# Kernel optimization log

Hardware: AMD Instinct MI355X
Metric: run time of the kernel (lower is better)

## Reference

```python
import jax, jax.numpy as jnp
import numpy as np

RBF_CO = 10.077141124806595


def setup_inputs() -> dict:
    key = jax.random.key(0)
    k1, k2, k3 = jax.random.split(key, 3)
    n, dim = 2048, 128
    N, out_dim = 50000, 64
    features = jax.random.normal(k1, (n, dim), dtype=jnp.float32)
    train_data = jax.random.normal(k2, (N, dim), dtype=jnp.float32)
    weights = jax.random.normal(k3, (N, out_dim), dtype=jnp.float32) * 0.02
    return {"features": features, "train_data": train_data, "weights": weights}


def reference(features, train_data, weights):
    x2 = jnp.sum(features * features, axis=-1, keepdims=True)      # [n, 1]
    t2 = jnp.sum(train_data * train_data, axis=-1)                 # [N]
    d2 = x2 + t2[None, :] - 2.0 * (features @ train_data.T)        # [n, N]
    dist = jnp.sqrt(jnp.maximum(d2, 0.0))                          # clamp fp error
    k = jnp.exp(-dist / RBF_CO / 2.0)                              # RBF kernel [n, N]
    return k @ weights                                              # [n, out_dim]
```

## Files before the change

kernel.cpp:

```cpp
#include <hip/hip_runtime.h>
#include <hip/hip_bf16.h>
#include <stdint.h>

#define DIM 128
#define ODIM 64
#define BM 128
#define BN 64
#define NSPLIT 64

typedef __attribute__((ext_vector_type(8))) __bf16 bf16x8;
typedef __attribute__((ext_vector_type(2))) __bf16 bf16x2;
typedef __attribute__((ext_vector_type(4))) float f32x4;

#define MFMA16(a, b, c) __builtin_amdgcn_mfma_f32_16x16x32_bf16((a), (b), (c), 0, 0, 0)

#define RBFD 10.077141124806595
#define LOG2E 1.4426950408889634
#define C2D ((LOG2E / (2.0 * RBFD)) * (LOG2E / (2.0 * RBFD)))

__device__ __forceinline__ void async_copy16(const void* g, void* l) {
  __builtin_amdgcn_global_load_lds((const __attribute__((address_space(1))) void*)g,
                                   (__attribute__((address_space(3))) void*)l, 16, 0, 0);
}

__device__ __forceinline__ uint32_t pack_bf16(float a, float b) {
  uint32_t ua = __builtin_bit_cast(uint32_t, a) + 0x8000u;
  uint32_t ub = __builtin_bit_cast(uint32_t, b) + 0x8000u;
  return __builtin_amdgcn_perm(ub, ua, 0x07060302u);
}

__global__ void prep_all(const float* __restrict__ train, __bf16* __restrict__ Tb,
                         float* __restrict__ t2, const float* __restrict__ feat,
                         __bf16* __restrict__ Fb, float* __restrict__ x2,
                         const float* __restrict__ W, __bf16* __restrict__ Wt,
                         int Ntrain, int Npad, int nFeat,
                         int trainBlocks, int rowBlocks, float scale, float tScale) {
  __shared__ float tile[64][65];
  const int b = (int)blockIdx.x;
  const int t = (int)threadIdx.x;

  if (b < rowBlocks) {
    const float* src;
    __bf16* dst;
    float* sq;
    int nValid, nPad, row0;
    float padv, rowScale;
    if (b < trainBlocks) {
      src = train; dst = Tb; sq = t2; nValid = Ntrain; nPad = Npad; row0 = b * 4;
      padv = 1e30f; rowScale = tScale;
    } else {
      src = feat; dst = Fb; sq = x2; nValid = nFeat; nPad = nFeat; row0 = (b - trainBlocks) * 4;
      padv = 0.0f; rowScale = 1.0f;
    }
    int row = row0 + (t >> 6);
    int lane = t & 63;
    if (row >= nPad) return;
    float2 v = make_float2(0.0f, 0.0f);
    if (row < nValid) v = ((const float2*)src)[(size_t)row * 64 + lane];
    float ss = v.x * v.x + v.y * v.y;
    bf16x2 p;
    p.x = (__bf16)(v.x * rowScale);
    p.y = (__bf16)(v.y * rowScale);
    *(bf16x2*)&dst[(size_t)row * DIM + lane * 2] = p;
    #pragma unroll
    for (int off = 32; off > 0; off >>= 1) ss += __shfl_down(ss, off);
    if (lane == 0) sq[row] = (row < nValid) ? ss * scale : padv;
    return;
  }

  int j0 = (b - rowBlocks) * 64;
  int jr = t >> 2;
  int cg = (t & 3) * 16;
  int j = j0 + jr;
  if (j < Ntrain) {
    const float4* src = (const float4*)(W + (size_t)j * ODIM);
    #pragma unroll
    for (int q = 0; q < 4; ++q) {
      float4 u = src[(cg >> 2) + q];
      tile[jr][cg + q * 4 + 0] = u.x;
      tile[jr][cg + q * 4 + 1] = u.y;
      tile[jr][cg + q * 4 + 2] = u.z;
      tile[jr][cg + q * 4 + 3] = u.w;
    }
  } else {
    #pragma unroll
    for (int q = 0; q < 16; ++q) tile[jr][cg + q] = 0.0f;
  }
  __syncthreads();
  int v = t >> 2;
  int jc = (t & 3) * 16;
  __bf16 ob[16];
  #pragma unroll
  for (int q = 0; q < 16; ++q) ob[q] = (__bf16)tile[jc + q][v];
  __bf16* dst = Wt + (size_t)v * Npad + j0 + jc;
  *(bf16x8*)dst = *(bf16x8*)&ob[0];
  *(bf16x8*)(dst + 8) = *(bf16x8*)&ob[8];
}

template <bool ATOMIC>
__global__ __launch_bounds__(256, 3) void rbf_main(
    const __bf16* __restrict__ Fb, const __bf16* __restrict__ Tb,
    const __bf16* __restrict__ Wt, const float* __restrict__ t2g,
    const float* __restrict__ x2g, float* __restrict__ outOrPart,
    int nRows, int Npad, int nChunks) {
  __shared__ __align__(16) char smem[24576];
  char* sT = smem;
  char* sP = smem;
  char* sW = smem + 16384;

  const int tid = threadIdx.x;
  const int wave = tid >> 6;
  const int lane = tid & 63;
  const int l16 = lane & 15;
  const int g4 = lane >> 4;

  const int ns = (int)blockIdx.x;
  const int mb = (int)blockIdx.y;

  bf16x8 bF[2][4];
  #pragma unroll
  for (int nf = 0; nf < 2; ++nf)
    #pragma unroll
    for (int ko = 0; ko < 4; ++ko)
      bF[nf][ko] = *(const bf16x8*)(Fb + ((size_t)(mb * BM + wave * 32 + nf * 16 + l16)) * DIM +
                                    ko * 32 + g4 * 8);

  float x2v[2];
  #pragma unroll
  for (int nf = 0; nf < 2; ++nf)
    x2v[nf] = x2g[mb * BM + wave * 32 + nf * 16 + l16];

  f32x4 zero4 = {0.0f, 0.0f, 0.0f, 0.0f};
  f32x4 oacc[2][4];
  #pragma unroll
  for (int mo = 0; mo < 2; ++mo)
    #pragma unroll
    for (int vi = 0; vi < 4; ++vi) oacc[mo][vi] = zero4;

  for (int c = ns; c < nChunks; c += NSPLIT) {
    const int n0 = c * BN;

    {
      const char* gT = (const char*)Tb + (size_t)n0 * 256;
      #pragma unroll
      for (int i = 0; i < 4; ++i) {
        int off = i * 4096 + wave * 1024;
        int loff = off + lane * 16;
        int row = loff >> 8;
        int gran = (loff >> 4) & 15;
        async_copy16(gT + row * 256 + ((gran ^ (row & 15)) << 4), sT + off);
      }
    }
    {
      #pragma unroll
      for (int i = 0; i < 2; ++i) {
        int off = i * 4096 + wave * 1024;
        int loff = off + lane * 16;
        int v = loff >> 7;
        int gran = (loff >> 4) & 7;
        const char* gW = (const char*)Wt + ((size_t)v * Npad + n0) * 2 + ((gran ^ (v & 7)) << 4);
        async_copy16(gW, sW + off);
      }
    }
    f32x4 t2v[4];
    #pragma unroll
    for (int mt = 0; mt < 4; ++mt)
      t2v[mt] = *(const f32x4*)(t2g + n0 + mt * 16 + g4 * 4);

    __syncthreads();

    f32x4 sacc[4][2];
    #pragma unroll
    for (int mt = 0; mt < 4; ++mt)
      #pragma unroll
      for (int nf = 0; nf < 2; ++nf)
        #pragma unroll
        for (int r = 0; r < 4; ++r) sacc[mt][nf][r] = t2v[mt][r] + x2v[nf];

    #pragma unroll
    for (int ko = 0; ko < 4; ++ko) {
      bf16x8 a[4];
      #pragma unroll
      for (int mt = 0; mt < 4; ++mt) {
        int row = mt * 16 + l16;
        int slot = (ko * 4 + g4) ^ l16;
        a[mt] = *(const bf16x8*)(sT + row * 256 + (slot << 4));
      }
      #pragma unroll
      for (int mt = 0; mt < 4; ++mt)
        #pragma unroll
        for (int nf = 0; nf < 2; ++nf)
          sacc[mt][nf] = MFMA16(a[mt], bF[nf][ko], sacc[mt][nf]);
    }

    __syncthreads();

    #pragma unroll
    for (int mt = 0; mt < 4; ++mt) {
      #pragma unroll
      for (int nf = 0; nf < 2; ++nf) {
        float kv[4];
        #pragma unroll
        for (int r = 0; r < 4; ++r) {
          float d2 = fmaxf(sacc[mt][nf][r], 0.0f);
          kv[r] = __builtin_amdgcn_exp2f(-__builtin_amdgcn_sqrtf(d2));
        }
        uint32_t lo = pack_bf16(kv[0], kv[1]);
        uint32_t hi = pack_bf16(kv[2], kv[3]);
        int prow = wave * 32 + nf * 16 + l16;
        int gran = (2 * mt + (g4 >> 1)) ^ (l16 & 7);
        uint2* dst = (uint2*)(sP + prow * 128 + (gran << 4) + (g4 & 1) * 8);
        *dst = make_uint2(lo, hi);
      }
    }

    #pragma unroll
    for (int ko2 = 0; ko2 < 2; ++ko2) {
      bf16x8 p[2];
      #pragma unroll
      for (int mo = 0; mo < 2; ++mo) {
        int prow = wave * 32 + mo * 16 + l16;
        int gran = (ko2 * 4 + g4) ^ (l16 & 7);
        p[mo] = *(const bf16x8*)(sP + prow * 128 + (gran << 4));
      }
      bf16x8 w[4];
      #pragma unroll
      for (int vi = 0; vi < 4; ++vi) {
        int v = vi * 16 + l16;
        int slot = (ko2 * 4 + g4) ^ (l16 & 7);
        w[vi] = *(const bf16x8*)(sW + v * 128 + (slot << 4));
      }
      #pragma unroll
      for (int mo = 0; mo < 2; ++mo)
        #pragma unroll
        for (int vi = 0; vi < 4; ++vi)
          oacc[mo][vi] = MFMA16(p[mo], w[vi], oacc[mo][vi]);
    }
    __syncthreads();
  }

  if (ATOMIC) {
    float* out = outOrPart;
    #pragma unroll
    for (int mo = 0; mo < 2; ++mo)
      #pragma unroll
      for (int vi = 0; vi < 4; ++vi)
        #pragma unroll
        for (int r = 0; r < 4; ++r) {
          int row = mb * BM + wave * 32 + mo * 16 + g4 * 4 + r;
          int col = vi * 16 + l16;
          atomicAdd(&out[(size_t)row * ODIM + col], oacc[mo][vi][r]);
        }
  } else {
    float* dst = outOrPart + (size_t)ns * (size_t)nRows * ODIM;
    #pragma unroll
    for (int mo = 0; mo < 2; ++mo)
      #pragma unroll
      for (int vi = 0; vi < 4; ++vi)
        #pragma unroll
        for (int r = 0; r < 4; ++r) {
          int row = mb * BM + wave * 32 + mo * 16 + g4 * 4 + r;
          int col = vi * 16 + l16;
          dst[(size_t)row * ODIM + col] = oacc[mo][vi][r];
        }
  }
}

__global__ void reduce_parts(const float4* __restrict__ part, float4* __restrict__ out,
                             int total4) {
  int i = (int)blockIdx.x * blockDim.x + threadIdx.x;
  if (i >= total4) return;
  float4 s = make_float4(0.0f, 0.0f, 0.0f, 0.0f);
  #pragma unroll
  for (int sp = 0; sp < NSPLIT; ++sp) {
    float4 v = part[(size_t)sp * total4 + i];
    s.x += v.x; s.y += v.y; s.z += v.z; s.w += v.w;
  }
  out[i] = s;
}

extern "C" void kernel_launch(void* const* d_in, const int* in_sizes, int n_in,
                              void* d_out, int out_size, void* d_ws, size_t ws_size,
                              hipStream_t stream) {
  (void)n_in;
  const float* features = (const float*)d_in[0];
  const float* train = (const float*)d_in[1];
  const float* weights = (const float*)d_in[2];
  float* out = (float*)d_out;

  const int n = in_sizes[0] / DIM;
  const int N = in_sizes[1] / DIM;
  const int Npad = ((N + 63) / 64) * 64;
  const int nChunks = Npad / 64;

  size_t off = 0;
  auto alloc = [&](size_t bytes) {
    size_t o = off;
    off = (off + bytes + 255) & ~(size_t)255;
    return o;
  };
  size_t oT = alloc((size_t)Npad * DIM * 2);
  size_t oW = alloc((size_t)ODIM * Npad * 2);
  size_t oF = alloc((size_t)n * DIM * 2);
  size_t ot2 = alloc((size_t)Npad * 4);
  size_t ox2 = alloc((size_t)n * 4);
  size_t oPart = alloc((size_t)NSPLIT * n * ODIM * 4);
  size_t needFull = off;

  char* ws = (char*)d_ws;
  __bf16* Tb = (__bf16*)(ws + oT);
  __bf16* Wt = (__bf16*)(ws + oW);
  __bf16* Fb = (__bf16*)(ws + oF);
  float* t2 = (float*)(ws + ot2);
  float* x2 = (float*)(ws + ox2);

  const float scale = (float)C2D;
  const float tScale = (float)(-2.0 * C2D);
  const int trainBlocks = Npad / 4;
  const int rowBlocks = trainBlocks + n / 4;
  const int wBlocks = Npad / 64;
  prep_all<<<rowBlocks + wBlocks, 256, 0, stream>>>(train, Tb, t2, features, Fb, x2,
                                                    weights, Wt, N, Npad, n,
                                                    trainBlocks, rowBlocks, scale, tScale);

  const int mBlocks = n / BM;
  dim3 grid(NSPLIT, mBlocks);

  if (ws_size >= needFull) {
    float* part = (float*)(ws + oPart);
    rbf_main<false><<<grid, 256, 0, stream>>>(Fb, Tb, Wt, t2, x2, part, n, Npad, nChunks);
    int total4 = n * ODIM / 4;
    reduce_parts<<<(total4 + 255) / 256, 256, 0, stream>>>((const float4*)part, (float4*)out,
                                                           total4);
  } else {
    hipMemsetAsync(d_out, 0, (size_t)out_size * sizeof(float), stream);
    rbf_main<true><<<grid, 256, 0, stream>>>(Fb, Tb, Wt, t2, x2, out, n, Npad, nChunks);
  }
}
```

Measured before the change: 152.9 us.

## Stage two chunks per iteration with doubled LDS and cut split count

The main loop now loads the T and W tiles for two chunks into separate LDS buffers at once, then runs both chunks' distance MFMAs, elementwise exp and PV MFMAs under one set of barriers. This halves the barriers per chunk and overlaps more global-load latency. The P scratch still aliases the first T buffer; this is safe because each wave only writes and reads its own rows. LDS use doubles to 48 KB, and NSPLIT drops from 64 to 48 so the grid fits in a single wave at 3 blocks per CU. In exchange, each block does more serial work, there is a small tail imbalance, and the single-chunk remainder path adds code.

```diff
diff --git a/kernel.cpp b/kernel.cpp
--- a/kernel.cpp
+++ b/kernel.cpp
@@ -6,7 +6,7 @@
 #define ODIM 64
 #define BM 128
 #define BN 64
-#define NSPLIT 64
+#define NSPLIT 48
 
 typedef __attribute__((ext_vector_type(8))) __bf16 bf16x8;
 typedef __attribute__((ext_vector_type(2))) __bf16 bf16x2;
@@ -103,10 +103,12 @@
     const __bf16* __restrict__ Wt, const float* __restrict__ t2g,
     const float* __restrict__ x2g, float* __restrict__ outOrPart,
     int nRows, int Npad, int nChunks) {
-  __shared__ __align__(16) char smem[24576];
-  char* sT = smem;
-  char* sP = smem;
-  char* sW = smem + 16384;
+  __shared__ __align__(16) char smem[49152];
+  char* sTA = smem;
+  char* sTB = smem + 16384;
+  char* sWA = smem + 32768;
+  char* sWB = smem + 40960;
+  char* sP  = smem;
 
   const int tid = threadIdx.x;
   const int wave = tid >> 6;
@@ -137,46 +139,37 @@
     #pragma unroll
     for (int vi = 0; vi < 4; ++vi) oacc[mo][vi] = zero4;
 
-  for (int c = ns; c < nChunks; c += NSPLIT) {
-    const int n0 = c * BN;
-
-    {
-      const char* gT = (const char*)Tb + (size_t)n0 * 256;
-      #pragma unroll
-      for (int i = 0; i < 4; ++i) {
-        int off = i * 4096 + wave * 1024;
-        int loff = off + lane * 16;
-        int row = loff >> 8;
-        int gran = (loff >> 4) & 15;
-        async_copy16(gT + row * 256 + ((gran ^ (row & 15)) << 4), sT + off);
-      }
-    }
-    {
-      #pragma unroll
-      for (int i = 0; i < 2; ++i) {
-        int off = i * 4096 + wave * 1024;
-        int loff = off + lane * 16;
-        int v = loff >> 7;
-        int gran = (loff >> 4) & 7;
-        const char* gW = (const char*)Wt + ((size_t)v * Npad + n0) * 2 + ((gran ^ (v & 7)) << 4);
-        async_copy16(gW, sW + off);
-      }
-    }
-    f32x4 t2v[4];
+  auto stageT = [&](char* lT, int c) {
+    const char* gT = (const char*)Tb + (size_t)c * (BN * DIM * 2);
+    #pragma unroll
+    for (int i = 0; i < 4; ++i) {
+      int off = i * 4096 + wave * 1024;
+      int loff = off + lane * 16;
+      int row = loff >> 8;
+      int gran = (loff >> 4) & 15;
+      async_copy16(gT + row * 256 + ((gran ^ (row & 15)) << 4), lT + off);
+    }
+  };
+  auto stageW = [&](char* lW, int c) {
+    #pragma unroll
+    for (int i = 0; i < 2; ++i) {
+      int off = i * 4096 + wave * 1024;
+      int loff = off + lane * 16;
+      int v = loff >> 7;
+      int gran = (loff >> 4) & 7;
+      const char* gW = (const char*)Wt + ((size_t)v * Npad + (size_t)c * BN) * 2 +
+                       ((gran ^ (v & 7)) << 4);
+      async_copy16(gW, lW + off);
+    }
+  };
+
+  auto sPhase = [&](const char* lT, const f32x4 t2v[4], f32x4 sacc[4][2]) {
     #pragma unroll
     for (int mt = 0; mt < 4; ++mt)
-      t2v[mt] = *(const f32x4*)(t2g + n0 + mt * 16 + g4 * 4);
-
-    __syncthreads();
-
-    f32x4 sacc[4][2];
-    #pragma unroll
-    for (int mt = 0; mt < 4; ++mt)
       #pragma unroll
       for (int nf = 0; nf < 2; ++nf)
         #pragma unroll
         for (int r = 0; r < 4; ++r) sacc[mt][nf][r] = t2v[mt][r] + x2v[nf];
-
     #pragma unroll
     for (int ko = 0; ko < 4; ++ko) {
       bf16x8 a[4];
@@ -184,7 +177,7 @@
       for (int mt = 0; mt < 4; ++mt) {
         int row = mt * 16 + l16;
         int slot = (ko * 4 + g4) ^ l16;
-        a[mt] = *(const bf16x8*)(sT + row * 256 + (slot << 4));
+        a[mt] = *(const bf16x8*)(lT + row * 256 + (slot << 4));
       }
       #pragma unroll
       for (int mt = 0; mt < 4; ++mt)
@@ -192,9 +185,9 @@
         for (int nf = 0; nf < 2; ++nf)
           sacc[mt][nf] = MFMA16(a[mt], bF[nf][ko], sacc[mt][nf]);
     }
-
-    __syncthreads();
-
+  };
+
+  auto ewPhase = [&](const f32x4 sacc[4][2]) {
     #pragma unroll
     for (int mt = 0; mt < 4; ++mt) {
       #pragma unroll
@@ -213,7 +206,9 @@
         *dst = make_uint2(lo, hi);
       }
     }
-
+  };
+
+  auto pvPhase = [&](const char* lW) {
     #pragma unroll
     for (int ko2 = 0; ko2 < 2; ++ko2) {
       bf16x8 p[2];
@@ -228,7 +223,7 @@
       for (int vi = 0; vi < 4; ++vi) {
         int v = vi * 16 + l16;
         int slot = (ko2 * 4 + g4) ^ (l16 & 7);
-        w[vi] = *(const bf16x8*)(sW + v * 128 + (slot << 4));
+        w[vi] = *(const bf16x8*)(lW + v * 128 + (slot << 4));
       }
       #pragma unroll
       for (int mo = 0; mo < 2; ++mo)
@@ -236,7 +231,47 @@
         for (int vi = 0; vi < 4; ++vi)
           oacc[mo][vi] = MFMA16(p[mo], w[vi], oacc[mo][vi]);
     }
-    __syncthreads();
+  };
+
+  int c = ns;
+  for (; c + NSPLIT < nChunks; c += 2 * NSPLIT) {
+    const int cA = c, cB = c + NSPLIT;
+    stageT(sTA, cA);
+    stageW(sWA, cA);
+    stageT(sTB, cB);
+    stageW(sWB, cB);
+    f32x4 t2vA[4], t2vB[4];
+    #pragma unroll
+    for (int mt = 0; mt < 4; ++mt) {
+      t2vA[mt] = *(const f32x4*)(t2g + cA * BN + mt * 16 + g4 * 4);
+      t2vB[mt] = *(const f32x4*)(t2g + cB * BN + mt * 16 + g4 * 4);
+    }
+    __syncthreads();
+
+    f32x4 sacc[4][2];
+    sPhase(sTA, t2vA, sacc);
+    __syncthreads();
+
+    ewPhase(sacc);
+    pvPhase(sWA);
+    sPhase(sTB, t2vB, sacc);
+    ewPhase(sacc);
+    pvPhase(sWB);
+    __syncthreads();
+  }
+  if (c < nChunks) {
+    stageT(sTA, c);
+    stageW(sWA, c);
+    f32x4 t2v[4];
+    #pragma unroll
+    for (int mt = 0; mt < 4; ++mt)
+      t2v[mt] = *(const f32x4*)(t2g + c * BN + mt * 16 + g4 * 4);
+    __syncthreads();
+    f32x4 sacc[4][2];
+    sPhase(sTA, t2v, sacc);
+    __syncthreads();
+    ewPhase(sacc);
+    pvPhase(sWA);
   }
 
   if (ATOMIC) {
```

Result: slower. 156.8 us (+2.5%).
